# Kernel tuning notes

Measured on AMD Instinct MI355X. Metric: run time of the kernel, lower is better.

The kernel has to match this reference:

```python
import jax, jax.numpy as jnp
import numpy as np

N = 30000          # nodes
R = 8              # relations
NUM_BASES = 30     # basis decomposition (fixed in module)
IN_DIM = 256
Z_DIM = 128
HID = Z_DIM * 2
E = N * 16         # edges (avg degree 16)


def setup_inputs() -> dict:
    key = jax.random.key(0)
    ks = jax.random.split(key, 12)
    x = jax.random.normal(ks[0], (N, IN_DIM), jnp.float32)
    edge_index = jax.random.randint(ks[1], (2, E), 0, N, dtype=jnp.int64)
    edge_type = jax.random.randint(ks[2], (E,), 0, R, dtype=jnp.int64)
    s1 = 1.0 / np.sqrt(IN_DIM)
    s2 = 1.0 / np.sqrt(HID)
    sb = 1.0 / np.sqrt(NUM_BASES)
    bases1 = jax.random.normal(ks[3], (NUM_BASES, IN_DIM, HID), jnp.float32) * s1
    comp1 = jax.random.normal(ks[4], (R, NUM_BASES), jnp.float32) * sb
    root1 = jax.random.normal(ks[5], (IN_DIM, HID), jnp.float32) * s1
    bias1 = jnp.zeros((HID,), jnp.float32)
    bases2 = jax.random.normal(ks[6], (NUM_BASES, HID, Z_DIM), jnp.float32) * s2
    comp2 = jax.random.normal(ks[7], (R, NUM_BASES), jnp.float32) * sb
    root2 = jax.random.normal(ks[8], (HID, Z_DIM), jnp.float32) * s2
    bias2 = jnp.zeros((Z_DIM,), jnp.float32)
    return dict(x=x, edge_index=edge_index, edge_type=edge_type,
                bases1=bases1, comp1=comp1, root1=root1, bias1=bias1,
                bases2=bases2, comp2=comp2, root2=root2, bias2=bias2)


def _rgcn_layer(x, src, dst, etype, bases, comp, root, bias):
    # weight[r] = sum_b comp[r,b] * bases[b]  (basis decomposition)
    n = x.shape[0]
    W = jnp.einsum('rb,bio->rio', comp, bases)          # [R, in, out]
    xall = jnp.einsum('ni,rio->nro', x, W)              # [N, R, out] dense transform
    msg = xall[src, etype]                              # [E, out] gather per edge
    seg = dst * R + etype                               # segment = (dst, relation)
    sums = jax.ops.segment_sum(msg, seg, num_segments=n * R)
    cnt = jax.ops.segment_sum(jnp.ones((msg.shape[0],), msg.dtype), seg,
                              num_segments=n * R)
    mean = sums / jnp.maximum(cnt, 1.0)[:, None]        # PyG RGCNConv aggr='mean'
    agg = mean.reshape(n, R, -1).sum(axis=1)            # sum over relations
    return agg + x @ root + bias


def reference(x, edge_index, edge_type, bases1, comp1, root1, bias1,
              bases2, comp2, root2, bias2):
    src, dst = edge_index[0], edge_index[1]
    z = _rgcn_layer(x, src, dst, edge_type, bases1, comp1, root1, bias1)
    z = jax.nn.leaky_relu(z, negative_slope=0.01)
    z = _rgcn_layer(z, src, dst, edge_type, bases2, comp2, root2, bias2)
    return z
```

## Files before the change

kernel.cpp:

```cpp
#include <hip/hip_runtime.h>
#include <hip/hip_bf16.h>
#include <stdint.h>

#define NN     30000
#define MPAD   30080
#define RR     8
#define NBASES 30
#define KD     256
#define EE     480000
#define NSEG   (NN * RR)
#define BK     64
#define CAP    32
#define NC1    2304
#define NC2    1152

typedef unsigned short u16;
typedef __attribute__((ext_vector_type(8))) short bf16x8;
typedef __attribute__((ext_vector_type(4))) float f32x4;

__device__ __forceinline__ u16 f2b(float f) {
  union { float f; uint32_t u; } v; v.f = f;
  return (u16)((v.u + 0x7fffu + ((v.u >> 16) & 1u)) >> 16);
}
__device__ __forceinline__ float b2f(u16 h) {
  union { uint32_t u; float f; } v; v.u = ((uint32_t)h) << 16;
  return v.f;
}

__device__ __forceinline__ void gl_lds16(const void* g, void* l) {
  __builtin_amdgcn_global_load_lds((__attribute__((address_space(1))) void*)g,
                                   (__attribute__((address_space(3))) void*)l,
                                   16, 0, 0);
}

template<int NCOLS>
__global__ __launch_bounds__(512, 2)
void k_gemm_y(const u16* __restrict__ A, const u16* __restrict__ Bn,
              u16* __restrict__ Y) {
  constexpr int NT = 128, MT = 128;
  constexpr int MI = 2, NI = 4;
  constexpr int NKI = KD / BK;
  __shared__ __align__(16) char smem[65536];
  u16 (*Alds)[MT * BK] = (u16(*)[MT * BK])smem;
  u16 (*Blds)[NT * BK] = (u16(*)[NT * BK])(smem + 2 * MT * BK * 2);
  float* eps = (float*)smem;
  const int tid = threadIdx.x;
  const int w = tid >> 6, lane = tid & 63;
  const int bn = blockIdx.x * NT, bm = blockIdx.y * MT;
  const int wm = (w >> 1) * 32;
  const int wn = (w & 1) * 64;
  const int l15 = lane & 15, l4 = lane >> 4;

  f32x4 acc[MI][NI];
  #pragma unroll
  for (int mi = 0; mi < MI; ++mi)
    #pragma unroll
    for (int ni = 0; ni < NI; ++ni) acc[mi][ni] = (f32x4){0.f, 0.f, 0.f, 0.f};

  auto stage = [&](int buf, int k0) {
    #pragma unroll
    for (int it = 0; it < 2; ++it) {
      int chb = it * 512 + w * 64;
      int ch = chb + lane;
      int row = ch >> 3, pc = ch & 7;
      int lc = pc ^ (row & 7);
      gl_lds16(&A[(size_t)(bm + row) * KD + k0 + lc * 8], &Alds[buf][chb * 8]);
    }
    #pragma unroll
    for (int it = 0; it < 2; ++it) {
      int chb = it * 512 + w * 64;
      int ch = chb + lane;
      int row = ch >> 3, pc = ch & 7;
      int lc = pc ^ (row & 7);
      gl_lds16(&Bn[(size_t)(bn + row) * KD + k0 + lc * 8], &Blds[buf][chb * 8]);
    }
  };

  stage(0, 0);
  __syncthreads();
  int buf = 0;
  for (int t = 0; t < NKI; ++t) {
    if (t + 1 < NKI) stage(buf ^ 1, (t + 1) * BK);
    #pragma unroll
    for (int s = 0; s < 2; ++s) {
      bf16x8 av[MI], bv[NI];
      #pragma unroll
      for (int mi = 0; mi < MI; ++mi) {
        int row = wm + mi * 16 + l15;
        int pc = (4 * s + l4) ^ (row & 7);
        av[mi] = *(const bf16x8*)&Alds[buf][row * BK + pc * 8];
      }
      #pragma unroll
      for (int ni = 0; ni < NI; ++ni) {
        int row = wn + ni * 16 + l15;
        int pc = (4 * s + l4) ^ (row & 7);
        bv[ni] = *(const bf16x8*)&Blds[buf][row * BK + pc * 8];
      }
      #pragma unroll
      for (int mi = 0; mi < MI; ++mi)
        #pragma unroll
        for (int ni = 0; ni < NI; ++ni)
          acc[mi][ni] = __builtin_amdgcn_mfma_f32_16x16x32_bf16(av[mi], bv[ni], acc[mi][ni], 0, 0, 0);
    }
    __syncthreads();
    buf ^= 1;
  }

  #pragma unroll
  for (int p = 0; p < 2; ++p) {
    if ((wm >> 6) == p) {
      #pragma unroll
      for (int mi = 0; mi < MI; ++mi)
        #pragma unroll
        for (int ni = 0; ni < NI; ++ni) {
          int col = wn + ni * 16 + l15;
          #pragma unroll
          for (int v = 0; v < 4; ++v) {
            int row = (wm & 63) + mi * 16 + l4 * 4 + v;
            eps[row * 132 + col] = acc[mi][ni][v];
          }
        }
    }
    __syncthreads();
    {
      int row = tid >> 3, oc = tid & 7;
      const float* src = &eps[row * 132 + oc * 16];
      uint4 o[2];
      #pragma unroll
      for (int hh = 0; hh < 2; ++hh) {
        float f0 = src[hh*8+0], f1 = src[hh*8+1], f2 = src[hh*8+2], f3 = src[hh*8+3];
        float f4 = src[hh*8+4], f5 = src[hh*8+5], f6 = src[hh*8+6], f7 = src[hh*8+7];
        o[hh].x = ((uint32_t)f2b(f1) << 16) | (uint32_t)f2b(f0);
        o[hh].y = ((uint32_t)f2b(f3) << 16) | (uint32_t)f2b(f2);
        o[hh].z = ((uint32_t)f2b(f5) << 16) | (uint32_t)f2b(f4);
        o[hh].w = ((uint32_t)f2b(f7) << 16) | (uint32_t)f2b(f6);
      }
      u16* dst = &Y[(size_t)(bm + p * 64 + row) * NCOLS + bn + oc * 16];
      *(uint4*)dst = o[0];
      *(uint4*)(dst + 8) = o[1];
    }
    __syncthreads();
  }
}

template<int D, bool LAST>
__global__ __launch_bounds__(256)
void k_agg(const u16* __restrict__ Y, const int* __restrict__ cnt,
           const int* __restrict__ esrc, const float* __restrict__ bias,
           u16* __restrict__ ob, float* __restrict__ of) {
  constexpr int YW = 9 * D;
  constexpr int CW = D / 32;
  const int tid = threadIdx.x;
  const int h = tid >> 5, ln = tid & 31;
  const int d = blockIdx.x * 8 + h;

  int cn[8];
  {
    int4 c0 = *(const int4*)&cnt[d << 3];
    int4 c1 = *(const int4*)&cnt[(d << 3) + 4];
    cn[0]=c0.x; cn[1]=c0.y; cn[2]=c0.z; cn[3]=c0.w;
    cn[4]=c1.x; cn[5]=c1.y; cn[6]=c1.z; cn[7]=c1.w;
  }
  int4 q[8];
  #pragma unroll
  for (int r = 0; r < 8; ++r)
    q[r] = *(const int4*)&esrc[((d << 3) + r) * CAP];

  float a[CW];
  #pragma unroll
  for (int j = 0; j < CW; ++j) a[j] = 0.f;

  #pragma unroll
  for (int r = 0; r < 8; ++r) {
    int n = cn[r] < CAP ? cn[r] : CAP;
    if (n == 0) continue;
    float t[CW];
    #pragma unroll
    for (int j = 0; j < CW; ++j) t[j] = 0.f;
    const int qsrc[4] = {q[r].x, q[r].y, q[r].z, q[r].w};
    #pragma unroll
    for (int e = 0; e < 4; ++e) {
      if (e < n) {
        int sr = qsrc[e];
        if constexpr (CW == 8) {
          uint4 v = *(const uint4*)&Y[(size_t)sr * YW + r * D + ln * 8];
          t[0]+=b2f((u16)v.x); t[1]+=b2f((u16)(v.x>>16));
          t[2]+=b2f((u16)v.y); t[3]+=b2f((u16)(v.y>>16));
          t[4]+=b2f((u16)v.z); t[5]+=b2f((u16)(v.z>>16));
          t[6]+=b2f((u16)v.w); t[7]+=b2f((u16)(v.w>>16));
        } else {
          uint2 v = *(const uint2*)&Y[(size_t)sr * YW + r * D + ln * 4];
          t[0]+=b2f((u16)v.x); t[1]+=b2f((u16)(v.x>>16));
          t[2]+=b2f((u16)v.y); t[3]+=b2f((u16)(v.y>>16));
        }
      }
    }
    #pragma unroll 1
    for (int e = 4; e < n; ++e) {
      int sr = esrc[((d << 3) + r) * CAP + e];
      if constexpr (CW == 8) {
        uint4 v = *(const uint4*)&Y[(size_t)sr * YW + r * D + ln * 8];
        t[0]+=b2f((u16)v.x); t[1]+=b2f((u16)(v.x>>16));
        t[2]+=b2f((u16)v.y); t[3]+=b2f((u16)(v.y>>16));
        t[4]+=b2f((u16)v.z); t[5]+=b2f((u16)(v.z>>16));
        t[6]+=b2f((u16)v.w); t[7]+=b2f((u16)(v.w>>16));
      } else {
        uint2 v = *(const uint2*)&Y[(size_t)sr * YW + r * D + ln * 4];
        t[0]+=b2f((u16)v.x); t[1]+=b2f((u16)(v.x>>16));
        t[2]+=b2f((u16)v.y); t[3]+=b2f((u16)(v.y>>16));
      }
    }
    float inv = 1.f / (float)n;
    #pragma unroll
    for (int j = 0; j < CW; ++j) a[j] = fmaf(inv, t[j], a[j]);
  }

  if constexpr (CW == 8) {
    uint4 sv = *(const uint4*)&Y[(size_t)d * YW + 8 * D + ln * 8];
    float s[8] = { b2f((u16)sv.x), b2f((u16)(sv.x>>16)),
                   b2f((u16)sv.y), b2f((u16)(sv.y>>16)),
                   b2f((u16)sv.z), b2f((u16)(sv.z>>16)),
                   b2f((u16)sv.w), b2f((u16)(sv.w>>16)) };
    float4 b0 = *(const float4*)&bias[ln * 8];
    float4 b1 = *(const float4*)&bias[ln * 8 + 4];
    float vv[8];
    vv[0]=a[0]+s[0]+b0.x; vv[1]=a[1]+s[1]+b0.y;
    vv[2]=a[2]+s[2]+b0.z; vv[3]=a[3]+s[3]+b0.w;
    vv[4]=a[4]+s[4]+b1.x; vv[5]=a[5]+s[5]+b1.y;
    vv[6]=a[6]+s[6]+b1.z; vv[7]=a[7]+s[7]+b1.w;
    if (!LAST) {
      #pragma unroll
      for (int j = 0; j < 8; ++j) vv[j] = vv[j] > 0.f ? vv[j] : 0.01f * vv[j];
      uint4 o;
      o.x = ((uint32_t)f2b(vv[1]) << 16) | (uint32_t)f2b(vv[0]);
      o.y = ((uint32_t)f2b(vv[3]) << 16) | (uint32_t)f2b(vv[2]);
      o.z = ((uint32_t)f2b(vv[5]) << 16) | (uint32_t)f2b(vv[4]);
      o.w = ((uint32_t)f2b(vv[7]) << 16) | (uint32_t)f2b(vv[6]);
      *(uint4*)&ob[(size_t)d * KD + ln * 8] = o;
    } else {
      float4 o0 = {vv[0], vv[1], vv[2], vv[3]};
      float4 o1 = {vv[4], vv[5], vv[6], vv[7]};
      *(float4*)&of[(size_t)d * 256 + ln * 8] = o0;
      *(float4*)&of[(size_t)d * 256 + ln * 8 + 4] = o1;
    }
  } else {
    uint2 sv = *(const uint2*)&Y[(size_t)d * YW + 8 * D + ln * 4];
    float s[4] = { b2f((u16)sv.x), b2f((u16)(sv.x>>16)),
                   b2f((u16)sv.y), b2f((u16)(sv.y>>16)) };
    float4 b0 = *(const float4*)&bias[ln * 4];
    float vv[4];
    vv[0]=a[0]+s[0]+b0.x; vv[1]=a[1]+s[1]+b0.y;
    vv[2]=a[2]+s[2]+b0.z; vv[3]=a[3]+s[3]+b0.w;
    if (!LAST) {
      #pragma unroll
      for (int j = 0; j < 4; ++j) vv[j] = vv[j] > 0.f ? vv[j] : 0.01f * vv[j];
      uint2 o;
      o.x = ((uint32_t)f2b(vv[1]) << 16) | (uint32_t)f2b(vv[0]);
      o.y = ((uint32_t)f2b(vv[3]) << 16) | (uint32_t)f2b(vv[2]);
      *(uint2*)&ob[(size_t)d * KD + ln * 4] = o;
    } else {
      float4 o = {vv[0], vv[1], vv[2], vv[3]};
      *(float4*)&of[(size_t)d * 128 + ln * 4] = o;
    }
  }
}

__global__ void k_cast_x(const float* __restrict__ x, u16* __restrict__ xb) {
  int t = blockIdx.x * 256 + threadIdx.x;
  if (t < NN * KD / 4) {
    float4 v = ((const float4*)x)[t];
    union { u16 h[4]; uint2 u; } p;
    p.h[0] = f2b(v.x); p.h[1] = f2b(v.y); p.h[2] = f2b(v.z); p.h[3] = f2b(v.w);
    ((uint2*)xb)[t] = p.u;
  }
}

__global__ void k_combineT1(const float* __restrict__ bases, const float* __restrict__ comp,
                            const float* __restrict__ root, u16* __restrict__ Bn) {
  int i = blockIdx.x, rg = blockIdx.y, o = threadIdx.x;
  float v; int j;
  if (rg < RR) {
    float acc = 0.f;
    #pragma unroll
    for (int b = 0; b < NBASES; ++b)
      acc += comp[rg * NBASES + b] * bases[(size_t)b * 65536 + i * 256 + o];
    v = acc; j = rg * 256 + o;
  } else {
    v = root[i * 256 + o]; j = 2048 + o;
  }
  Bn[(size_t)j * KD + i] = f2b(v);
}

__global__ void k_combineT2(const float* __restrict__ bases, const float* __restrict__ comp,
                            const float* __restrict__ root, u16* __restrict__ Bn) {
  int i = blockIdx.x, rg = blockIdx.y, o = threadIdx.x;
  float v; int j;
  if (rg < RR) {
    float acc = 0.f;
    #pragma unroll
    for (int b = 0; b < NBASES; ++b)
      acc += comp[rg * NBASES + b] * bases[(size_t)b * 32768 + i * 128 + o];
    v = acc; j = rg * 128 + o;
  } else {
    v = root[i * 128 + o]; j = 1024 + o;
  }
  Bn[(size_t)j * KD + i] = f2b(v);
}

__global__ void k_bucket_fs(const int* __restrict__ ei, const int* __restrict__ ety,
                            int* __restrict__ cnt, int* __restrict__ esrc) {
  int e = blockIdx.x * 256 + threadIdx.x;
  if (e < EE) {
    int seg = ei[EE + e] * RR + ety[e];
    int pos = atomicAdd(&cnt[seg], 1);
    if (pos < CAP) esrc[seg * CAP + pos] = ei[e];
  }
}

extern "C" void kernel_launch(void* const* d_in, const int* in_sizes, int n_in,
                              void* d_out, int out_size, void* d_ws, size_t ws_size,
                              hipStream_t stream) {
  const float* x      = (const float*)d_in[0];
  const int*   ei     = (const int*)d_in[1];
  const int*   ety    = (const int*)d_in[2];
  const float* bases1 = (const float*)d_in[3];
  const float* comp1  = (const float*)d_in[4];
  const float* root1  = (const float*)d_in[5];
  const float* bias1  = (const float*)d_in[6];
  const float* bases2 = (const float*)d_in[7];
  const float* comp2  = (const float*)d_in[8];
  const float* root2  = (const float*)d_in[9];
  const float* bias2  = (const float*)d_in[10];
  float* out = (float*)d_out;

  char* p = (char*)d_ws;
  auto alloc = [&](size_t bytes) {
    char* q = p; p += (bytes + 255) & ~(size_t)255; return q;
  };
  u16* Y    = (u16*)alloc((size_t)MPAD * NC1 * 2);
  u16* xb   = (u16*)alloc((size_t)MPAD * KD * 2);
  u16* z1b  = (u16*)alloc((size_t)MPAD * KD * 2);
  u16* Bn1  = (u16*)alloc((size_t)NC1 * KD * 2);
  u16* Bn2  = (u16*)alloc((size_t)NC2 * KD * 2);
  int* cnt  = (int*)alloc((size_t)NSEG * 4);
  int* esrc = (int*)alloc((size_t)NSEG * CAP * 4);

  hipMemsetAsync(cnt, 0, (size_t)NSEG * 4, stream);
  k_bucket_fs<<<(EE + 255) / 256, 256, 0, stream>>>(ei, ety, cnt, esrc);

  k_cast_x<<<NN * KD / 4 / 256, 256, 0, stream>>>(x, xb);
  k_combineT1<<<dim3(256, 9), 256, 0, stream>>>(bases1, comp1, root1, Bn1);
  k_combineT2<<<dim3(256, 9), 128, 0, stream>>>(bases2, comp2, root2, Bn2);

  k_gemm_y<NC1><<<dim3(NC1 / 128, MPAD / 128), 512, 0, stream>>>(xb, Bn1, Y);
  k_agg<256, false><<<NN / 8, 256, 0, stream>>>(Y, cnt, esrc, bias1, z1b, nullptr);

  k_gemm_y<NC2><<<dim3(NC2 / 128, MPAD / 128), 512, 0, stream>>>(z1b, Bn2, Y);
  k_agg<128, true><<<NN / 8, 256, 0, stream>>>(Y, cnt, esrc, bias2, nullptr, out);
}
```

Measured before the change: 347.5 us.

## Pin full-K B tile in LDS and loop over M tiles per block

Replaces the double-buffered K-loop GEMM with a kernel that loads a 128x256 B tile into LDS once per block. Each block then iterates over five 128-row A tiles, prefetching the next A tile into registers while the current one is computed, which cuts redundant B reloads and per-tile launch overhead. The LDS-staged, vectorized bf16 epilogue is replaced by direct scalar nontemporal 2-byte stores. The risks are weaker write coalescing on the large Y output and lower occupancy from the 128KB LDS footprint per block.

```diff
diff --git a/kernel.cpp b/kernel.cpp
--- a/kernel.cpp
+++ b/kernel.cpp
@@ -9,7 +9,6 @@
 #define KD     256
 #define EE     480000
 #define NSEG   (NN * RR)
-#define BK     64
 #define CAP    32
 #define NC1    2304
 #define NC2    1152
@@ -35,111 +34,102 @@
 
 template<int NCOLS>
 __global__ __launch_bounds__(512, 2)
-void k_gemm_y(const u16* __restrict__ A, const u16* __restrict__ Bn,
-              u16* __restrict__ Y) {
-  constexpr int NT = 128, MT = 128;
-  constexpr int MI = 2, NI = 4;
-  constexpr int NKI = KD / BK;
-  __shared__ __align__(16) char smem[65536];
-  u16 (*Alds)[MT * BK] = (u16(*)[MT * BK])smem;
-  u16 (*Blds)[NT * BK] = (u16(*)[NT * BK])(smem + 2 * MT * BK * 2);
-  float* eps = (float*)smem;
+void k_gemm_bpin(const u16* __restrict__ A, const u16* __restrict__ Bn,
+                 u16* __restrict__ Y) {
+  constexpr int MIT = 5;
+  __shared__ u16 Blds[128 * 256];
+  __shared__ u16 Alds[128 * 256];
   const int tid = threadIdx.x;
   const int w = tid >> 6, lane = tid & 63;
-  const int bn = blockIdx.x * NT, bm = blockIdx.y * MT;
+  const int bn = blockIdx.x * 128;
+  const int bm0 = blockIdx.y * (MIT * 128);
   const int wm = (w >> 1) * 32;
   const int wn = (w & 1) * 64;
   const int l15 = lane & 15, l4 = lane >> 4;
 
-  f32x4 acc[MI][NI];
   #pragma unroll
-  for (int mi = 0; mi < MI; ++mi)
-    #pragma unroll
-    for (int ni = 0; ni < NI; ++ni) acc[mi][ni] = (f32x4){0.f, 0.f, 0.f, 0.f};
-
-  auto stage = [&](int buf, int k0) {
-    #pragma unroll
-    for (int it = 0; it < 2; ++it) {
-      int chb = it * 512 + w * 64;
-      int ch = chb + lane;
-      int row = ch >> 3, pc = ch & 7;
-      int lc = pc ^ (row & 7);
-      gl_lds16(&A[(size_t)(bm + row) * KD + k0 + lc * 8], &Alds[buf][chb * 8]);
-    }
-    #pragma unroll
-    for (int it = 0; it < 2; ++it) {
-      int chb = it * 512 + w * 64;
-      int ch = chb + lane;
-      int row = ch >> 3, pc = ch & 7;
-      int lc = pc ^ (row & 7);
-      gl_lds16(&Bn[(size_t)(bn + row) * KD + k0 + lc * 8], &Blds[buf][chb * 8]);
+  for (int it = 0; it < 8; ++it) {
+    int sb = it * 512 + w * 64;
+    int s = sb + lane;
+    int row = s >> 5, c = s & 31;
+    int lc = c ^ (row & 7);
+    gl_lds16(&Bn[(size_t)(bn + row) * KD + lc * 8], &Blds[sb * 8]);
+  }
+
+  uint4 ar[8];
+  auto aload = [&](int bm) {
+    #pragma unroll
+    for (int j = 0; j < 8; ++j) {
+      int s = j * 512 + tid;
+      int row = s >> 5, c = s & 31;
+      int lc = c ^ (row & 7);
+      ar[j] = *(const uint4*)&A[(size_t)(bm + row) * KD + lc * 8];
     }
   };
-
-  stage(0, 0);
+  auto awrite = [&]() {
+    #pragma unroll
+    for (int j = 0; j < 8; ++j) {
+      int s = j * 512 + tid;
+      *(uint4*)&Alds[s * 8] = ar[j];
+    }
+  };
+
+  aload(bm0);
   __syncthreads();
-  int buf = 0;
-  for (int t = 0; t < NKI; ++t) {
-    if (t + 1 < NKI) stage(buf ^ 1, (t + 1) * BK);
-    #pragma unroll
-    for (int s = 0; s < 2; ++s) {
-      bf16x8 av[MI], bv[NI];
-      #pragma unroll
-      for (int mi = 0; mi < MI; ++mi) {
+  awrite();
+  asm volatile("s_waitcnt lgkmcnt(0)" ::: "memory");
+  __builtin_amdgcn_s_barrier();
+
+  for (int t = 0; t < MIT; ++t) {
+    const int bm = bm0 + t * 128;
+    if (t + 1 < MIT) aload(bm + 128);
+
+    f32x4 acc[2][4];
+    #pragma unroll
+    for (int mi = 0; mi < 2; ++mi)
+      #pragma unroll
+      for (int ni = 0; ni < 4; ++ni) acc[mi][ni] = (f32x4){0.f, 0.f, 0.f, 0.f};
+
+    #pragma unroll
+    for (int ks = 0; ks < 8; ++ks) {
+      bf16x8 av[2], bv[4];
+      #pragma unroll
+      for (int mi = 0; mi < 2; ++mi) {
         int row = wm + mi * 16 + l15;
-        int pc = (4 * s + l4) ^ (row & 7);
-        av[mi] = *(const bf16x8*)&Alds[buf][row * BK + pc * 8];
-      }
-      #pragma unroll
-      for (int ni = 0; ni < NI; ++ni) {
+        av[mi] = *(const bf16x8*)&Alds[row * 256 + ((4 * ks + l4) ^ (row & 7)) * 8];
+      }
+      #pragma unroll
+      for (int ni = 0; ni < 4; ++ni) {
         int row = wn + ni * 16 + l15;
-        int pc = (4 * s + l4) ^ (row & 7);
-        bv[ni] = *(const bf16x8*)&Blds[buf][row * BK + pc * 8];
-      }
-      #pragma unroll
-      for (int mi = 0; mi < MI; ++mi)
+        bv[ni] = *(const bf16x8*)&Blds[row * 256 + ((4 * ks + l4) ^ (row & 7)) * 8];
+      }
+      #pragma unroll
+      for (int mi = 0; mi < 2; ++mi)
         #pragma unroll
-        for (int ni = 0; ni < NI; ++ni)
+        for (int ni = 0; ni < 4; ++ni)
           acc[mi][ni] = __builtin_amdgcn_mfma_f32_16x16x32_bf16(av[mi], bv[ni], acc[mi][ni], 0, 0, 0);
     }
-    __syncthreads();
-    buf ^= 1;
-  }
-
-  #pragma unroll
-  for (int p = 0; p < 2; ++p) {
-    if ((wm >> 6) == p) {
-      #pragma unroll
-      for (int mi = 0; mi < MI; ++mi)
+
+    #pragma unroll
+    for (int mi = 0; mi < 2; ++mi)
+      #pragma unroll
+      for (int ni = 0; ni < 4; ++ni) {
+        int col = bn + wn + ni * 16 + l15;
+        int rbase = bm + wm + mi * 16 + l4 * 4;
         #pragma unroll
-        for (int ni = 0; ni < NI; ++ni) {
-          int col = wn + ni * 16 + l15;
-          #pragma unroll
-          for (int v = 0; v < 4; ++v) {
-            int row = (wm & 63) + mi * 16 + l4 * 4 + v;
-            eps[row * 132 + col] = acc[mi][ni][v];
-          }
+        for (int v = 0; v < 4; ++v) {
+          u16 hv = f2b(acc[mi][ni][v]);
+          __builtin_nontemporal_store(hv, &Y[(size_t)(rbase + v) * NCOLS + col]);
         }
-    }
-    __syncthreads();
-    {
-      int row = tid >> 3, oc = tid & 7;
-      const float* src = &eps[row * 132 + oc * 16];
-      uint4 o[2];
-      #pragma unroll
-      for (int hh = 0; hh < 2; ++hh) {
-        float f0 = src[hh*8+0], f1 = src[hh*8+1], f2 = src[hh*8+2], f3 = src[hh*8+3];
-        float f4 = src[hh*8+4], f5 = src[hh*8+5], f6 = src[hh*8+6], f7 = src[hh*8+7];
-        o[hh].x = ((uint32_t)f2b(f1) << 16) | (uint32_t)f2b(f0);
-        o[hh].y = ((uint32_t)f2b(f3) << 16) | (uint32_t)f2b(f2);
-        o[hh].z = ((uint32_t)f2b(f5) << 16) | (uint32_t)f2b(f4);
-        o[hh].w = ((uint32_t)f2b(f7) << 16) | (uint32_t)f2b(f6);
-      }
-      u16* dst = &Y[(size_t)(bm + p * 64 + row) * NCOLS + bn + oc * 16];
-      *(uint4*)dst = o[0];
-      *(uint4*)(dst + 8) = o[1];
-    }
-    __syncthreads();
+      }
+
+    asm volatile("" ::: "memory");
+    __builtin_amdgcn_s_barrier();
+    if (t + 1 < MIT) {
+      awrite();
+      asm volatile("s_waitcnt lgkmcnt(0)" ::: "memory");
+    }
+    __builtin_amdgcn_s_barrier();
   }
 }
 
@@ -352,9 +342,9 @@
   k_combineT1<<<dim3(256, 9), 256, 0, stream>>>(bases1, comp1, root1, Bn1);
   k_combineT2<<<dim3(256, 9), 128, 0, stream>>>(bases2, comp2, root2, Bn2);
 
-  k_gemm_y<NC1><<<dim3(NC1 / 128, MPAD / 128), 512, 0, stream>>>(xb, Bn1, Y);
+  k_gemm_bpin<NC1><<<dim3(NC1 / 128, 47), 512, 0, stream>>>(xb, Bn1, Y);
   k_agg<256, false><<<NN / 8, 256, 0, stream>>>(Y, cnt, esrc, bias1, z1b, nullptr);
 
-  k_gemm_y<NC2><<<dim3(NC2 / 128, MPAD / 128), 512, 0, stream>>>(z1b, Bn2, Y);
+  k_gemm_bpin<NC2><<<dim3(NC2 / 128, 47), 512, 0, stream>>>(z1b, Bn2, Y);
   k_agg<128, true><<<NN / 8, 256, 0, stream>>>(Y, cnt, esrc, bias2, nullptr, out);
 }
```

Measured after the change: 465.4 us. +33.9%, slower.
